# Kernel optimization log

Hardware: AMD Instinct MI355X
Metric: run time of the kernel (lower is better)

The kernel has to match this reference:

```python
import jax, jax.numpy as jnp
import numpy as np


def _make_stencil():
    # Fixed finite-difference kernels from the torch module __init__
    w = np.zeros((4, 1, 3, 3), np.float32)
    w[0, 0, 1, 1] = 1.0; w[0, 0, 1, 2] = -1.0   # self - right
    w[1, 0, 1, 0] = 1.0; w[1, 0, 1, 1] = -1.0   # left - self
    w[2, 0, 1, 1] = 1.0; w[2, 0, 2, 1] = -1.0   # self - down
    w[3, 0, 0, 1] = 1.0; w[3, 0, 1, 1] = -1.0   # up - self
    return jnp.asarray(w)


def setup_inputs() -> dict:
    key = jax.random.key(0)
    H, W, S = 2160, 3840, 512
    seg = jax.random.randint(key, (1, 1, H, W), 0, S, dtype=jnp.int32)
    return {"seg": seg, "w": _make_stencil(), "num_segments": S}


def reference(seg, w, num_segments):
    S = int(num_segments)
    H, W_ = seg.shape[2], seg.shape[3]
    x = seg.astype(jnp.float32)
    # Conv2d(padding=3, padding_mode='replicate'): edge-pad by 3 then VALID 3x3 conv
    xp = jnp.pad(x, ((0, 0), (0, 0), (3, 3), (3, 3)), mode='edge')
    res = jax.lax.conv_general_dilated(
        xp, w, window_strides=(1, 1), padding='VALID',
        dimension_numbers=('NCHW', 'OIHW', 'NCHW'))  # (1,4,H+4,W+4)
    bm = (res != 0)[0, :, 2:-2, 2:-2]  # (4,H,W); boundary masks per direction

    s2 = seg[0, 0]  # (H,W) int
    # In the torch code, the k-th True of mask0 at (y,x) pairs with the k-th True
    # of mask1 at (y,x+1) (mask1 is mask0 shifted by +1 in x; replicate padding
    # guarantees equal counts). Hence horizontal edges are (seg[y,x], seg[y,x+1])
    # where bm[0], and vertical edges (seg[y,x], seg[y+1,x]) where bm[2].
    right_nb = jnp.concatenate([s2[:, 1:], s2[:, -1:]], axis=1)
    down_nb = jnp.concatenate([s2[1:, :], s2[-1:, :]], axis=0)

    flat = s2.ravel()
    adj = jnp.zeros((S, S), jnp.float32)
    adj = adj.at[flat, right_nb.ravel()].add(bm[0].astype(jnp.float32).ravel())
    adj = adj.at[flat, down_nb.ravel()].add(bm[2].astype(jnp.float32).ravel())
    # unique pairs -> presence matrix; diagonal (self-pairs) never occurs in original
    adj = jnp.where(adj > 0, 1.0, 0.0) * (1.0 - jnp.eye(S, dtype=jnp.float32))

    # centers(): per-segment mean of (x_index, y_index) -- the torch permute
    # reverses dims so column 0 is the W-axis mean, column 1 the H-axis mean.
    ys = jnp.broadcast_to(jnp.arange(H, dtype=jnp.float32)[:, None], (H, W_)).ravel()
    xs = jnp.broadcast_to(jnp.arange(W_, dtype=jnp.float32)[None, :], (H, W_)).ravel()
    cnt = jax.ops.segment_sum(jnp.ones_like(xs), flat, num_segments=S)
    sx = jax.ops.segment_sum(xs, flat, num_segments=S)
    sy = jax.ops.segment_sum(ys, flat, num_segments=S)
    centers = jnp.stack([sx, sy], axis=1) / cnt[:, None]
    return adj, centers
```

## Files before the change

### kernel.cpp

```cpp
#include <hip/hip_runtime.h>

#define HH 2160
#define WW 3840
#define SS 512
#define NW (SS * SS / 32)
#define NBMAX 512

typedef unsigned int uint;
typedef unsigned long long ull;

__global__ __launch_bounds__(512) void seg_main(
    const int* __restrict__ seg, uint* __restrict__ wsBm,
    uint* __restrict__ part, int nb) {
  __shared__ uint s_bm[NW];
  __shared__ ull  s_pk[SS];
  __shared__ uint s_sx[SS];
  for (int i = threadIdx.x; i < NW; i += blockDim.x) s_bm[i] = 0u;
  for (int i = threadIdx.x; i < SS; i += blockDim.x) { s_pk[i] = 0ULL; s_sx[i] = 0u; }
  __syncthreads();

  const int NC = HH * WW / 4;
  const int stride = gridDim.x * blockDim.x;
  const int4* __restrict__ seg4  = (const int4*)seg;
  const int4* __restrict__ seg4d = (const int4*)(seg + WW);

  for (int c = blockIdx.x * blockDim.x + threadIdx.x; c < NC; c += stride) {
    const int p = c * 4;
    const int y = p / WW;
    const int x = p - y * WW;
    const int4 v = seg4[c];
    const int4 d = (y < HH - 1) ? seg4d[c] : v;
    const int nxt = (x < WW - 4) ? seg[p + 4] : v.w;

    if (v.x != v.y) { int i = v.x * SS + v.y; atomicOr(&s_bm[i >> 5], 1u << (i & 31)); }
    if (v.y != v.z) { int i = v.y * SS + v.z; atomicOr(&s_bm[i >> 5], 1u << (i & 31)); }
    if (v.z != v.w) { int i = v.z * SS + v.w; atomicOr(&s_bm[i >> 5], 1u << (i & 31)); }
    if (v.w != nxt) { int i = v.w * SS + nxt; atomicOr(&s_bm[i >> 5], 1u << (i & 31)); }
    if (v.x != d.x) { int i = v.x * SS + d.x; atomicOr(&s_bm[i >> 5], 1u << (i & 31)); }
    if (v.y != d.y) { int i = v.y * SS + d.y; atomicOr(&s_bm[i >> 5], 1u << (i & 31)); }
    if (v.z != d.z) { int i = v.z * SS + d.z; atomicOr(&s_bm[i >> 5], 1u << (i & 31)); }
    if (v.w != d.w) { int i = v.w * SS + d.w; atomicOr(&s_bm[i >> 5], 1u << (i & 31)); }

    const ull yp = (1ULL << 40) | (ull)(uint)y;
    atomicAdd(&s_pk[v.x], yp); atomicAdd(&s_sx[v.x], (uint)x);
    atomicAdd(&s_pk[v.y], yp); atomicAdd(&s_sx[v.y], (uint)(x + 1));
    atomicAdd(&s_pk[v.z], yp); atomicAdd(&s_sx[v.z], (uint)(x + 2));
    atomicAdd(&s_pk[v.w], yp); atomicAdd(&s_sx[v.w], (uint)(x + 3));
  }
  __syncthreads();

  uint* myBm = wsBm + (size_t)blockIdx.x * NW;
  for (int i = threadIdx.x; i < NW; i += blockDim.x) myBm[i] = s_bm[i];

  for (int i = threadIdx.x; i < SS; i += blockDim.x) {
    const ull pk = s_pk[i];
    part[(0 * SS + i) * nb + blockIdx.x] = (uint)(pk >> 40);
    part[(1 * SS + i) * nb + blockIdx.x] = s_sx[i];
    part[(2 * SS + i) * nb + blockIdx.x] = (uint)(pk & ((1ULL << 40) - 1));
  }
}

__global__ __launch_bounds__(256) void finalize(
    const uint* __restrict__ wsBm, const uint* __restrict__ part, int nb,
    float* __restrict__ adj, float* __restrict__ centers) {
  const int g = blockIdx.x;
  const int t = threadIdx.x;

  if (g < SS) {
    const int k  = t & 15;
    const int bg = t >> 4;
    uint acc = 0u;
    const uint* base = wsBm + g * 16 + k;
    for (int b = bg; b < nb; b += 16) acc |= base[(size_t)b * NW];

    __shared__ uint s_red[16][16];
    __shared__ uint s_word[16];
    s_red[bg][k] = acc;
    __syncthreads();
    if (t < 16) {
      uint w = 0u;
      #pragma unroll
      for (int i = 0; i < 16; i++) w |= s_red[i][t];
      s_word[t] = w;
    }
    __syncthreads();
    if (t < 128) {
      const int cell = t * 4;
      const uint nib = (s_word[cell >> 5] >> (cell & 31)) & 0xFu;
      float4 q;
      q.x = (nib & 1u) ? 1.0f : 0.0f;
      q.y = (nib & 2u) ? 1.0f : 0.0f;
      q.z = (nib & 4u) ? 1.0f : 0.0f;
      q.w = (nib & 8u) ? 1.0f : 0.0f;
      ((float4*)(adj + g * SS))[t] = q;
    }
  } else {
    const int s = (g - SS) * 64 + (t >> 2);
    const int q = t & 3;
    ull cnt = 0, sx = 0, sy = 0;
    for (int b = q; b < nb; b += 4) {
      cnt += part[(0 * SS + s) * nb + b];
      sx  += part[(1 * SS + s) * nb + b];
      sy  += part[(2 * SS + s) * nb + b];
    }
    cnt += __shfl_down(cnt, 2, 4); cnt += __shfl_down(cnt, 1, 4);
    sx  += __shfl_down(sx,  2, 4); sx  += __shfl_down(sx,  1, 4);
    sy  += __shfl_down(sy,  2, 4); sy  += __shfl_down(sy,  1, 4);
    if (q == 0) {
      const double dc = (double)cnt;
      centers[s * 2 + 0] = (float)((double)sx / dc);
      centers[s * 2 + 1] = (float)((double)sy / dc);
    }
  }
}

extern "C" void kernel_launch(void* const* d_in, const int* in_sizes, int n_in,
                              void* d_out, int out_size, void* d_ws, size_t ws_size,
                              hipStream_t stream) {
  const int* seg = (const int*)d_in[0];
  float* out = (float*)d_out;
  float* adj = out;
  float* centers = out + SS * SS;

  int nb = NBMAX;
  const size_t per_block = (size_t)(NW + 3 * SS) * sizeof(uint);
  if (ws_size < (size_t)nb * per_block) {
    nb = (int)(ws_size / per_block);
    if (nb > NBMAX) nb = NBMAX;
    if (nb < 1) nb = 1;
  }
  uint* wsBm = (uint*)d_ws;
  uint* part = wsBm + (size_t)nb * NW;

  seg_main<<<nb, 512, 0, stream>>>(seg, wsBm, part, nb);
  finalize<<<SS + 8, 256, 0, stream>>>(wsBm, part, nb, adj, centers);
}
```

Measured before the change: 124.9 us.

## Merge per-block bitmaps via global atomicOr and pack centroid sums into one atomic

```diff
diff --git a/kernel.cpp b/kernel.cpp
--- a/kernel.cpp
+++ b/kernel.cpp
@@ -4,33 +4,40 @@
 #define WW 3840
 #define SS 512
 #define NW (SS * SS / 32)
-#define NBMAX 512
+#define NB 512
 
 typedef unsigned int uint;
 typedef unsigned long long ull;
 
 __global__ __launch_bounds__(512) void seg_main(
-    const int* __restrict__ seg, uint* __restrict__ wsBm,
+    const int* __restrict__ seg, uint* __restrict__ wsOr,
     uint* __restrict__ part, int nb) {
   __shared__ uint s_bm[NW];
   __shared__ ull  s_pk[SS];
-  __shared__ uint s_sx[SS];
-  for (int i = threadIdx.x; i < NW; i += blockDim.x) s_bm[i] = 0u;
-  for (int i = threadIdx.x; i < SS; i += blockDim.x) { s_pk[i] = 0ULL; s_sx[i] = 0u; }
+  for (int i = threadIdx.x; i < NW; i += 512) s_bm[i] = 0u;
+  for (int i = threadIdx.x; i < SS; i += 512) s_pk[i] = 0ULL;
   __syncthreads();
 
-  const int NC = HH * WW / 4;
-  const int stride = gridDim.x * blockDim.x;
+  const int NC  = HH * WW / 4;
+  const int cpb = (NC + nb - 1) / nb;
+  const int c0  = blockIdx.x * cpb;
+  const int c1  = min(c0 + cpb, NC);
+  const int y0  = (c0 * 4) / WW;
+  const int lane = threadIdx.x & 63;
+
   const int4* __restrict__ seg4  = (const int4*)seg;
   const int4* __restrict__ seg4d = (const int4*)(seg + WW);
 
-  for (int c = blockIdx.x * blockDim.x + threadIdx.x; c < NC; c += stride) {
+  for (int c = c0 + threadIdx.x; c < c1; c += 512) {
     const int p = c * 4;
     const int y = p / WW;
     const int x = p - y * WW;
     const int4 v = seg4[c];
     const int4 d = (y < HH - 1) ? seg4d[c] : v;
-    const int nxt = (x < WW - 4) ? seg[p + 4] : v.w;
+    const int nshfl = __shfl_down(v.x, 1, 64);
+    const bool need_load = (lane == 63) || (c + 1 >= c1);
+    const int  a4 = min(p + 4, HH * WW - 1);
+    const int  nxt = (x >= WW - 4) ? v.w : (need_load ? seg[a4] : nshfl);
 
     if (v.x != v.y) { int i = v.x * SS + v.y; atomicOr(&s_bm[i >> 5], 1u << (i & 31)); }
     if (v.y != v.z) { int i = v.y * SS + v.z; atomicOr(&s_bm[i >> 5], 1u << (i & 31)); }
@@ -41,61 +48,46 @@
     if (v.z != d.z) { int i = v.z * SS + d.z; atomicOr(&s_bm[i >> 5], 1u << (i & 31)); }
     if (v.w != d.w) { int i = v.w * SS + d.w; atomicOr(&s_bm[i >> 5], 1u << (i & 31)); }
 
-    const ull yp = (1ULL << 40) | (ull)(uint)y;
-    atomicAdd(&s_pk[v.x], yp); atomicAdd(&s_sx[v.x], (uint)x);
-    atomicAdd(&s_pk[v.y], yp); atomicAdd(&s_sx[v.y], (uint)(x + 1));
-    atomicAdd(&s_pk[v.z], yp); atomicAdd(&s_sx[v.z], (uint)(x + 2));
-    atomicAdd(&s_pk[v.w], yp); atomicAdd(&s_sx[v.w], (uint)(x + 3));
+    const ull yp = (1ULL << 48) | ((ull)(uint)x << 20) | (ull)(uint)(y - y0);
+    atomicAdd(&s_pk[v.x], yp);
+    atomicAdd(&s_pk[v.y], yp + (1ULL << 20));
+    atomicAdd(&s_pk[v.z], yp + (2ULL << 20));
+    atomicAdd(&s_pk[v.w], yp + (3ULL << 20));
   }
   __syncthreads();
 
-  uint* myBm = wsBm + (size_t)blockIdx.x * NW;
-  for (int i = threadIdx.x; i < NW; i += blockDim.x) myBm[i] = s_bm[i];
-
-  for (int i = threadIdx.x; i < SS; i += blockDim.x) {
+  for (int i = threadIdx.x; i < NW; i += 512) {
+    const uint m = s_bm[i];
+    if (m) atomicOr(&wsOr[i], m);
+  }
+  for (int i = threadIdx.x; i < SS; i += 512) {
     const ull pk = s_pk[i];
-    part[(0 * SS + i) * nb + blockIdx.x] = (uint)(pk >> 40);
-    part[(1 * SS + i) * nb + blockIdx.x] = s_sx[i];
-    part[(2 * SS + i) * nb + blockIdx.x] = (uint)(pk & ((1ULL << 40) - 1));
+    const uint cnt = (uint)(pk >> 48);
+    const uint sx  = (uint)((pk >> 20) & 0x0FFFFFFFu);
+    const uint sy  = (uint)(pk & 0xFFFFFu) + cnt * (uint)y0;
+    part[(0 * SS + i) * nb + blockIdx.x] = cnt;
+    part[(1 * SS + i) * nb + blockIdx.x] = sx;
+    part[(2 * SS + i) * nb + blockIdx.x] = sy;
   }
 }
 
 __global__ __launch_bounds__(256) void finalize(
-    const uint* __restrict__ wsBm, const uint* __restrict__ part, int nb,
+    const uint* __restrict__ wsOr, const uint* __restrict__ part, int nb,
     float* __restrict__ adj, float* __restrict__ centers) {
   const int g = blockIdx.x;
   const int t = threadIdx.x;
 
-  if (g < SS) {
-    const int k  = t & 15;
-    const int bg = t >> 4;
-    uint acc = 0u;
-    const uint* base = wsBm + g * 16 + k;
-    for (int b = bg; b < nb; b += 16) acc |= base[(size_t)b * NW];
-
-    __shared__ uint s_red[16][16];
-    __shared__ uint s_word[16];
-    s_red[bg][k] = acc;
-    __syncthreads();
-    if (t < 16) {
-      uint w = 0u;
-      #pragma unroll
-      for (int i = 0; i < 16; i++) w |= s_red[i][t];
-      s_word[t] = w;
-    }
-    __syncthreads();
-    if (t < 128) {
-      const int cell = t * 4;
-      const uint nib = (s_word[cell >> 5] >> (cell & 31)) & 0xFu;
-      float4 q;
-      q.x = (nib & 1u) ? 1.0f : 0.0f;
-      q.y = (nib & 2u) ? 1.0f : 0.0f;
-      q.z = (nib & 4u) ? 1.0f : 0.0f;
-      q.w = (nib & 8u) ? 1.0f : 0.0f;
-      ((float4*)(adj + g * SS))[t] = q;
-    }
+  if (g < 256) {
+    const int q4 = g * 256 + t;
+    const uint nib = (wsOr[q4 >> 3] >> ((q4 & 7) * 4)) & 0xFu;
+    float4 o;
+    o.x = (nib & 1u) ? 1.0f : 0.0f;
+    o.y = (nib & 2u) ? 1.0f : 0.0f;
+    o.z = (nib & 4u) ? 1.0f : 0.0f;
+    o.w = (nib & 8u) ? 1.0f : 0.0f;
+    ((float4*)adj)[q4] = o;
   } else {
-    const int s = (g - SS) * 64 + (t >> 2);
+    const int s = (g - 256) * 64 + (t >> 2);
     const int q = t & 3;
     ull cnt = 0, sx = 0, sy = 0;
     for (int b = q; b < nb; b += 4) {
@@ -122,16 +114,18 @@
   float* adj = out;
   float* centers = out + SS * SS;
 
-  int nb = NBMAX;
-  const size_t per_block = (size_t)(NW + 3 * SS) * sizeof(uint);
-  if (ws_size < (size_t)nb * per_block) {
-    nb = (int)(ws_size / per_block);
-    if (nb > NBMAX) nb = NBMAX;
-    if (nb < 1) nb = 1;
+  uint* wsOr = (uint*)d_ws;
+  uint* part = wsOr + NW;
+
+  int nb = NB;
+  const size_t need = (size_t)NW * 4 + (size_t)3 * SS * nb * 4;
+  if (ws_size < need) {
+    nb = (int)((ws_size - (size_t)NW * 4) / ((size_t)3 * SS * 4));
+    if (nb > NB) nb = NB;
+    if (nb < 256) nb = 256;
   }
-  uint* wsBm = (uint*)d_ws;
-  uint* part = wsBm + (size_t)nb * NW;
 
-  seg_main<<<nb, 512, 0, stream>>>(seg, wsBm, part, nb);
-  finalize<<<SS + 8, 256, 0, stream>>>(wsBm, part, nb, adj, centers);
+  hipMemsetAsync(wsOr, 0, (size_t)NW * 4, stream);
+  seg_main<<<nb, 512, 0, stream>>>(seg, wsOr, part, nb);
+  finalize<<<256 + SS / 64, 256, 0, stream>>>(wsOr, part, nb, adj, centers);
 }
```

Result: slower. 132.3 us (+5.9%).
